# Performance work log

Hardware: AMD Instinct MI355X
Metric: run time of the kernel (lower is better)

## Reference

```python
import jax, jax.numpy as jnp
import numpy as np


def setup_inputs() -> dict:
    key = jax.random.key(0)
    k1, k2, k3, k4 = jax.random.split(key, 4)
    B, Cin, Cout, K, Wd, H, Wsp = 16, 256, 256, 3, 256, 64, 64
    fan_in = Cin * K * K
    return {
        "x": jax.random.normal(k1, (B, Cin, H, Wsp), dtype=jnp.float32),
        "w": jax.random.normal(k2, (B, Wd), dtype=jnp.float32),
        "conv_weight": jax.random.normal(k3, (Cout, Cin, K, K), dtype=jnp.float32) * 0.05,
        "style_w": jax.random.normal(k4, (Cin, Wd), dtype=jnp.float32) * 0.05,
        "style_b": jnp.zeros((Cin,), dtype=jnp.float32),
        "scale": jnp.asarray(1.0 / np.sqrt(fan_in), dtype=jnp.float32),
    }


def reference(x, w, conv_weight, style_w, style_b, scale):
    # x: [B, Cin, H, W]; w: [B, Wd]; conv_weight: [Cout, Cin, K, K]
    B, Cin, H, Wsp = x.shape
    Cout, _, K, _ = conv_weight.shape
    # style modulation: s = Linear(w) -> [B, 1, Cin, 1, 1]
    s = (w @ style_w.T + style_b).reshape(B, 1, Cin, 1, 1)
    # modulate + demodulate per-sample weights: [B, Cout, Cin, K, K]
    wt = (conv_weight * scale)[None] * s
    demod = jax.lax.rsqrt(jnp.sum(wt * wt, axis=(2, 3, 4), keepdims=True) + 1e-8)
    wt = (wt * demod).reshape(B * Cout, Cin, K, K)
    # grouped conv emulation: input [1, B*Cin, H, W], groups=B
    xr = x.reshape(1, B * Cin, H, Wsp)
    pad = 1
    out = jax.lax.conv_general_dilated(
        xr, wt,
        window_strides=(1, 1),
        padding=[(pad, pad), (pad, pad)],
        dimension_numbers=("NCHW", "OIHW", "NCHW"),
        feature_group_count=B,
    )
    return out.reshape(B, Cout, out.shape[2], out.shape[3])
```

## Files before the change

kernel.cpp:

```cpp
#include <hip/hip_runtime.h>
#include <hip/hip_bf16.h>

#define BB   16
#define CIN  256
#define COUT 256
#define WD   256
#define HH   64
#define WWS  64
#define NSP  4096
#define KW   9

typedef __attribute__((ext_vector_type(8))) short short8;
typedef __attribute__((ext_vector_type(4))) float f32x4;
typedef unsigned short ushort_t;
typedef unsigned int uint_t;

#define S_BYTES (BB*CIN*4)
#define WT_OFF (S_BYTES)
#define WT_BYTES (BB*9*COUT*CIN*2)
#define X_OFF (WT_OFF + WT_BYTES)
#define X_BYTES (BB*NSP*CIN*2)
#define ZP_OFF (X_OFF + X_BYTES)
#define ZP_BYTES 4096
#define WS_NEEDED ((size_t)(ZP_OFF + ZP_BYTES))

#define WAITVM0 asm volatile("s_waitcnt vmcnt(0)" ::: "memory")
#define WAITVM2 asm volatile("s_waitcnt vmcnt(2)" ::: "memory")

__device__ inline ushort_t f2bf(float f) {
    __hip_bfloat16 h = __float2bfloat16(f);
    return __builtin_bit_cast(ushort_t, h);
}

__device__ inline void gload_lds16(const ushort_t* g, ushort_t* l) {
    __builtin_amdgcn_global_load_lds(
        (const __attribute__((address_space(1))) void*)g,
        (__attribute__((address_space(3))) void*)l, 16, 0, 0);
}

__global__ __launch_bounds__(256)
void style_kernel(const float* __restrict__ w,
                  const float* __restrict__ style_w,
                  const float* __restrict__ style_b,
                  float* __restrict__ s) {
    const int b  = blockIdx.x;
    const int ci = threadIdx.x;
    __shared__ float wsh[WD];
    wsh[ci] = w[b * WD + ci];
    __syncthreads();
    const float* row = style_w + ci * WD;
    float acc = style_b[ci];
    #pragma unroll 4
    for (int k = 0; k < WD; ++k) acc += wsh[k] * row[k];
    s[b * CIN + ci] = acc;
}

__global__ __launch_bounds__(256)
void wt_kernel(const float* __restrict__ cw, const float* __restrict__ s,
               const float* __restrict__ scale_p, ushort_t* __restrict__ wt,
               float* __restrict__ zp) {
    const int co = blockIdx.x, b = blockIdx.y, ci = threadIdx.x;
    if (co == 0 && b == 0)
        ((float4*)zp)[ci] = make_float4(0.f, 0.f, 0.f, 0.f);
    const float sv = s[b * CIN + ci] * scale_p[0];
    const float* cp = cw + ((size_t)co * CIN + ci) * KW;
    float v[9];
    float ss = 0.f;
    #pragma unroll
    for (int t = 0; t < 9; ++t) { v[t] = cp[t] * sv; ss += v[t] * v[t]; }
    #pragma unroll
    for (int off = 32; off > 0; off >>= 1) ss += __shfl_down(ss, off);
    __shared__ float red[4];
    if ((ci & 63) == 0) red[ci >> 6] = ss;
    __syncthreads();
    const float dm = rsqrtf(red[0] + red[1] + red[2] + red[3] + 1e-8f);
    #pragma unroll
    for (int t = 0; t < 9; ++t)
        wt[((size_t)(b * 9 + t) * COUT + co) * CIN + ci] = f2bf(v[t] * dm);
}

__global__ __launch_bounds__(256)
void xpose_kernel(const float* __restrict__ x, ushort_t* __restrict__ xo) {
    const int spt = blockIdx.x;
    const int cit = blockIdx.y;
    const int b   = blockIdx.z;
    const int t   = threadIdx.x;
    __shared__ ushort_t tile[64 * 72];
    const int sp0 = spt * 64, ci0 = cit * 64;
    {
        const int spq = t & 15, cil = t >> 4;
        #pragma unroll
        for (int i = 0; i < 4; ++i) {
            const int ci = cil + i * 16;
            const float4 v = *(const float4*)(x + ((size_t)(b * CIN + ci0 + ci)) * NSP + sp0 + spq * 4);
            tile[(spq * 4 + 0) * 72 + ci] = f2bf(v.x);
            tile[(spq * 4 + 1) * 72 + ci] = f2bf(v.y);
            tile[(spq * 4 + 2) * 72 + ci] = f2bf(v.z);
            tile[(spq * 4 + 3) * 72 + ci] = f2bf(v.w);
        }
    }
    __syncthreads();
    {
        const int g8 = t & 7, sp = t >> 3;
        #pragma unroll
        for (int i = 0; i < 2; ++i) {
            const int spp = sp + i * 32;
            uint4 v = *(const uint4*)&tile[spp * 72 + g8 * 8];
            *(uint4*)(xo + ((size_t)(b * NSP + sp0 + spp)) * CIN + ci0 + g8 * 8) = v;
        }
    }
}

__global__ __launch_bounds__(256, 2)
void conv_mfma_kernel(const ushort_t* __restrict__ wt,
                      const ushort_t* __restrict__ xo,
                      const ushort_t* __restrict__ zp,
                      float* __restrict__ out) {
    const int wg     = blockIdx.x;
    const int b      = (wg & 7) | (((wg >> 3) & 1) << 3);
    const int cohalf = (wg >> 4) & 1;
    const int ntile  = wg >> 5;
    const int y0     = ntile * 4;

    const int tid  = threadIdx.x;
    const int lane = tid & 63;
    const int w    = tid >> 6;
    const int wm   = w >> 1;
    const int wn   = w & 1;
    const int wn2  = wn * 2;
    const int l15  = lane & 15;
    const int lg   = lane >> 4;

    __shared__ __align__(16) ushort_t lds_x[6 * 66 * 64];
    __shared__ __align__(16) ushort_t lds_a[3 * 128 * 32];

    const int srcqA = ((tid & 3) ^ ((tid >> 2) & 3)) * 8;
    const ushort_t* paDMA = wt + (size_t)b * (9 * COUT * CIN)
                          + (uint_t)(cohalf * 128 + (tid >> 2)) * CIN + srcqA;
    const ushort_t* xob = xo + (size_t)b * (NSP * CIN);

    const int sA8   = (lg ^ (l15 & 3)) * 8;
    const int abase = (wm * 64 + l15) * 32 + sA8;

    f32x4 acc[4][8];
    #pragma unroll
    for (int mi = 0; mi < 4; ++mi)
        #pragma unroll
        for (int ni = 0; ni < 8; ++ni) acc[mi][ni] = (f32x4){0.f, 0.f, 0.f, 0.f};

    if (tid < 96) {
        const int cell = tid >> 3;
        const int r = cell >> 1, c = (cell & 1) * 65;
        *(uint4*)&lds_x[(r * 66 + c) * 64 + (tid & 7) * 8] =
            make_uint4(0, 0, 0, 0);
    }

    #define STAGE_X(qt)                                                        \
    {   _Pragma("unroll")                                                      \
        for (int i_ = 0; i_ < 12; ++i_) {                                      \
            const int cell_ = i_ * 4 + w;                           \
            const int r_  = cell_ >> 3;                              \
            const int c0_ = 1 + (cell_ & 7) * 8;                               \
            const int y_  = y0 - 1 + r_;                                       \
            const int c_  = c0_ + (lane >> 3);                                 \
            const int qq_ = (lane & 7) ^ (c_ & 7);                             \
            const ushort_t* src_ = (y_ >= 0 && y_ < HH)                        \
                ? (xob + (uint_t)(y_ * WWS + c_ - 1) * CIN + (qt) * 64         \
                       + qq_ * 8)                                              \
                : (zp + lane * 8);                                             \
            gload_lds16(src_, lds_x + (r_ * 66 + c0_) * 64 + lane * 8);        \
        }                                                                      \
    }

    #define TAPB(ch2, t, BX, QB, QN)                                           \
    {                                                                          \
        WAITVM2;                          \
        __builtin_amdgcn_sched_barrier(0);                                     \
        __builtin_amdgcn_s_barrier();          \
        {                                 \
            const int lt2_ = (ch2) * 9 + (t) + 2;                              \
            const int tp_  = (lt2_ < 18) ? (lt2_ % 9) : (lt2_ - 18);           \
            const int cg_  = (lt2_ < 18) ? ((QB) + lt2_ / 9) : (QN);           \
            const uint_t ao_ = (uint_t)tp_ * 65536u + (uint_t)cg_ * 32u;       \
            ushort_t* ad_ = lds_a + (lt2_ % 3) * 4096 + tid * 8;               \
            gload_lds16(paDMA + ao_, ad_);                                     \
            gload_lds16(paDMA + 16384 + ao_, ad_ + 2048);                      \
        }                                                                      \
        const int ky_ = (t) / 3, kx_ = (t) % 3;                                \
        const ushort_t* ab_ = lds_a + (((ch2) * 9 + (t)) % 3) * 4096 + abase;  \
        short8 af_[4];                                                         \
        _Pragma("unroll")                                                      \
        for (int mi_ = 0; mi_ < 4; ++mi_)                                      \
            af_[mi_] = *(const short8*)(ab_ + mi_ * 512);                      \
        short8 bf_[8];                                                         \
        _Pragma("unroll")                                                      \
        for (int ni_ = 0; ni_ < 8; ++ni_)                                      \
            bf_[ni_] = *(const short8*)(lds_x + BX[kx_]                        \
                        + (((ni_ >> 2) + ky_) * 66) * 64 + (ni_ & 3) * 1024);  \
        __builtin_amdgcn_s_setprio(1);                                         \
        _Pragma("unroll")                                                      \
        for (int mi_ = 0; mi_ < 4; ++mi_)                                      \
            _Pragma("unroll")                                                  \
            for (int ni_ = 0; ni_ < 8; ++ni_)                                  \
                acc[mi_][ni_] = __builtin_amdgcn_mfma_f32_16x16x32_bf16(       \
                    bf_[ni_], af_[mi_], acc[mi_][ni_], 0, 0, 0);               \
        __builtin_amdgcn_s_setprio(0);                                         \
        __builtin_amdgcn_sched_barrier(0);                                     \
    }

    STAGE_X(0);
    gload_lds16(paDMA, lds_a + tid * 8);
    gload_lds16(paDMA + 16384, lds_a + 2048 + tid * 8);
    gload_lds16(paDMA + 65536, lds_a + 4096 + tid * 8);
    gload_lds16(paDMA + 65536 + 16384, lds_a + 6144 + tid * 8);
    WAITVM0;
    asm volatile("s_waitcnt lgkmcnt(0)" ::: "memory");
    __builtin_amdgcn_sched_barrier(0);
    __builtin_amdgcn_s_barrier();

    #pragma unroll 1
    for (int qt = 0; qt < 4; ++qt) {
        if (qt) {
            asm volatile("s_waitcnt lgkmcnt(0)" ::: "memory");
            __builtin_amdgcn_sched_barrier(0);
            __builtin_amdgcn_s_barrier();
            STAGE_X(qt);
            WAITVM0;
            __builtin_amdgcn_sched_barrier(0);
            __builtin_amdgcn_s_barrier();
        }
        const int qb = qt * 2;
        const int qn = ((qt + 1) & 3) * 2;

        int bx0[3], bx1[3];
        #pragma unroll
        for (int kx = 0; kx < 3; ++kx) {
            const int colb = (wn2 * 66 + l15 + kx) * 64;
            const int k7   = (l15 + kx) & 7;
            bx0[kx] = colb + ((0 + lg) ^ k7) * 8;
            bx1[kx] = colb + ((4 + lg) ^ k7) * 8;
        }

        TAPB(0,0,bx0,qb,qn) TAPB(0,1,bx0,qb,qn) TAPB(0,2,bx0,qb,qn)
        TAPB(0,3,bx0,qb,qn) TAPB(0,4,bx0,qb,qn) TAPB(0,5,bx0,qb,qn)
        TAPB(0,6,bx0,qb,qn) TAPB(0,7,bx0,qb,qn) TAPB(0,8,bx0,qb,qn)
        TAPB(1,0,bx1,qb,qn) TAPB(1,1,bx1,qb,qn) TAPB(1,2,bx1,qb,qn)
        TAPB(1,3,bx1,qb,qn) TAPB(1,4,bx1,qb,qn) TAPB(1,5,bx1,qb,qn)
        TAPB(1,6,bx1,qb,qn) TAPB(1,7,bx1,qb,qn) TAPB(1,8,bx1,qb,qn)
    }
    #undef TAPB
    #undef STAGE_X

    asm volatile("s_waitcnt vmcnt(0) lgkmcnt(0)" ::: "memory");
    __builtin_amdgcn_sched_barrier(0);

    #pragma unroll
    for (int mi = 0; mi < 4; ++mi) {
        const int co = cohalf * 128 + wm * 64 + mi * 16 + l15;
        float* ob = out + ((size_t)(b * COUT + co)) * NSP
                  + ntile * 256 + wn * 128 + lg * 4;
        #pragma unroll
        for (int ni = 0; ni < 8; ++ni)
            *(f32x4*)(ob + (ni >> 2) * 64 + (ni & 3) * 16) = acc[mi][ni];
    }
}

__global__ __launch_bounds__(256)
void modconv_kernel(const float* __restrict__ x,
                    const float* __restrict__ cw,
                    const float* __restrict__ s,
                    const float* __restrict__ scale_p,
                    float* __restrict__ out) {
    const int tile = blockIdx.x;
    const int co   = blockIdx.y;
    const int b    = blockIdx.z;
    const int tid  = threadIdx.x;
    const float scale = scale_p[0];

    __shared__ float s_wt[CIN * KW];
    __shared__ float s_x[18 * 66];
    __shared__ float red[4];

    const float* cwb = cw + (size_t)co * CIN * KW;
    const float* sb  = s + b * CIN;
    float sumsq = 0.f;
    for (int i = tid; i < CIN * KW; i += 256) {
        float v = cwb[i] * scale * sb[i / KW];
        s_wt[i] = v;
        sumsq += v * v;
    }
    #pragma unroll
    for (int off = 32; off > 0; off >>= 1) sumsq += __shfl_down(sumsq, off);
    if ((tid & 63) == 0) red[tid >> 6] = sumsq;
    __syncthreads();
    const float demod = rsqrtf(red[0] + red[1] + red[2] + red[3] + 1e-8f);
    for (int i = tid; i < CIN * KW; i += 256) s_wt[i] *= demod;

    const int tx = tid & 63;
    const int tr = tid >> 6;
    const int y0 = tile * 16;
    float acc[4] = {0.f, 0.f, 0.f, 0.f};

    for (int ci = 0; ci < CIN; ++ci) {
        __syncthreads();
        const float* xb = x + ((size_t)(b * CIN + ci)) * (HH * WWS);
        for (int idx = tid; idx < 18 * 66; idx += 256) {
            const int r = idx / 66, c = idx % 66;
            const int yg = y0 - 1 + r, xg = c - 1;
            float v = 0.f;
            if (yg >= 0 && yg < HH && xg >= 0 && xg < WWS) v = xb[yg * WWS + xg];
            s_x[idx] = v;
        }
        __syncthreads();
        const float* wr = s_wt + ci * KW;
        const float w0 = wr[0], w1 = wr[1], w2 = wr[2];
        const float w3 = wr[3], w4 = wr[4], w5 = wr[5];
        const float w6 = wr[6], w7 = wr[7], w8 = wr[8];
        const int rbase = tr * 4;
        float xv[6][3];
        #pragma unroll
        for (int j = 0; j < 6; ++j)
            #pragma unroll
            for (int k = 0; k < 3; ++k) xv[j][k] = s_x[(rbase + j) * 66 + tx + k];
        #pragma unroll
        for (int i = 0; i < 4; ++i)
            acc[i] += w0 * xv[i][0] + w1 * xv[i][1] + w2 * xv[i][2]
                    + w3 * xv[i+1][0] + w4 * xv[i+1][1] + w5 * xv[i+1][2]
                    + w6 * xv[i+2][0] + w7 * xv[i+2][1] + w8 * xv[i+2][2];
    }
    float* ob = out + (((size_t)(b * COUT + co)) * HH + y0) * WWS + tx;
    #pragma unroll
    for (int i = 0; i < 4; ++i) ob[(tr * 4 + i) * WWS] = acc[i];
}

extern "C" void kernel_launch(void* const* d_in, const int* in_sizes, int n_in,
                              void* d_out, int out_size, void* d_ws, size_t ws_size,
                              hipStream_t stream) {
    const float* x       = (const float*)d_in[0];
    const float* w       = (const float*)d_in[1];
    const float* cw      = (const float*)d_in[2];
    const float* style_w = (const float*)d_in[3];
    const float* style_b = (const float*)d_in[4];
    const float* scale_p = (const float*)d_in[5];
    float*       out     = (float*)d_out;

    float*    s    = (float*)d_ws;
    ushort_t* wswt = (ushort_t*)((char*)d_ws + WT_OFF);
    ushort_t* wsx  = (ushort_t*)((char*)d_ws + X_OFF);
    float*    zp   = (float*)((char*)d_ws + ZP_OFF);

    style_kernel<<<dim3(BB), 256, 0, stream>>>(w, style_w, style_b, s);

    if (ws_size >= WS_NEEDED) {
        wt_kernel<<<dim3(COUT, BB), 256, 0, stream>>>(cw, s, scale_p, wswt, zp);
        xpose_kernel<<<dim3(64, 4, BB), 256, 0, stream>>>(x, wsx);
        conv_mfma_kernel<<<dim3(512), 256, 0, stream>>>(wswt, wsx,
                                                        (const ushort_t*)zp, out);
    } else {
        modconv_kernel<<<dim3(4, COUT, BB), 256, 0, stream>>>(x, cw, s, scale_p, out);
    }
}
```

Before: 109.8 us.

## Widen conv tile to all 256 output channels and double-buffer LDS fragment reads

Each workgroup now computes all 256 output channels for its spatial tile instead of half of them. This halves the grid to 256 blocks and doubles the per-wave accumulator tile to 8x8 MFMA fragments, so each staged input tile is reused across twice as many channels and is no longer loaded twice. A and B fragments are register double-buffered, so reads for the next tap are issued before the current tap's MFMAs. The weight DMA is issued before the wait, with the vmcnt threshold raised to match the larger loads. The costs are much higher register pressure (launch bounds drop to one block per CU), lower occupancy, and fewer workgroups than a 256-CU device can fill with more than one block each.

```diff
diff --git a/kernel.cpp b/kernel.cpp
--- a/kernel.cpp
+++ b/kernel.cpp
@@ -25,7 +25,7 @@
 #define WS_NEEDED ((size_t)(ZP_OFF + ZP_BYTES))
 
 #define WAITVM0 asm volatile("s_waitcnt vmcnt(0)" ::: "memory")
-#define WAITVM2 asm volatile("s_waitcnt vmcnt(2)" ::: "memory")
+#define WAITVM4 asm volatile("s_waitcnt vmcnt(4)" ::: "memory")
 
 __device__ inline ushort_t f2bf(float f) {
     __hip_bfloat16 h = __float2bfloat16(f);
@@ -111,16 +111,15 @@
     }
 }
 
-__global__ __launch_bounds__(256, 2)
+__global__ __launch_bounds__(256, 1)
 void conv_mfma_kernel(const ushort_t* __restrict__ wt,
                       const ushort_t* __restrict__ xo,
                       const ushort_t* __restrict__ zp,
                       float* __restrict__ out) {
-    const int wg     = blockIdx.x;
-    const int b      = (wg & 7) | (((wg >> 3) & 1) << 3);
-    const int cohalf = (wg >> 4) & 1;
-    const int ntile  = wg >> 5;
-    const int y0     = ntile * 4;
+    const int wg    = blockIdx.x;
+    const int b     = (wg & 7) | (((wg >> 3) & 1) << 3);
+    const int ntile = wg >> 4;
+    const int y0    = ntile * 4;
 
     const int tid  = threadIdx.x;
     const int lane = tid & 63;
@@ -132,21 +131,32 @@
     const int lg   = lane >> 4;
 
     __shared__ __align__(16) ushort_t lds_x[6 * 66 * 64];
-    __shared__ __align__(16) ushort_t lds_a[3 * 128 * 32];
+    __shared__ __align__(16) ushort_t lds_a[3 * 256 * 32];
 
     const int srcqA = ((tid & 3) ^ ((tid >> 2) & 3)) * 8;
     const ushort_t* paDMA = wt + (size_t)b * (9 * COUT * CIN)
-                          + (uint_t)(cohalf * 128 + (tid >> 2)) * CIN + srcqA;
+                          + (uint_t)(tid >> 2) * CIN + srcqA;
     const ushort_t* xob = xo + (size_t)b * (NSP * CIN);
 
     const int sA8   = (lg ^ (l15 & 3)) * 8;
-    const int abase = (wm * 64 + l15) * 32 + sA8;
-
-    f32x4 acc[4][8];
-    #pragma unroll
-    for (int mi = 0; mi < 4; ++mi)
+    const int abase = (wm * 128 + l15) * 32 + sA8;
+
+    int bx[2][3];
+    #pragma unroll
+    for (int c4 = 0; c4 < 2; ++c4)
+        #pragma unroll
+        for (int kx = 0; kx < 3; ++kx) {
+            const int k7 = (l15 + kx) & 7;
+            bx[c4][kx] = (wn2 * 66 + l15 + kx) * 64 + ((c4 * 4 + lg) ^ k7) * 8;
+        }
+
+    f32x4 acc[8][8];
+    #pragma unroll
+    for (int mi = 0; mi < 8; ++mi)
         #pragma unroll
         for (int ni = 0; ni < 8; ++ni) acc[mi][ni] = (f32x4){0.f, 0.f, 0.f, 0.f};
+
+    short8 afr[2][8], bfr[2][8];
 
     if (tid < 96) {
         const int cell = tid >> 3;
@@ -172,91 +182,106 @@
         }                                                                      \
     }
 
-    #define TAPB(ch2, t, BX, QB, QN)                                           \
+    #define ISSUE_A(tp, cg, buf)                                               \
+    {   const ushort_t* as_ = paDMA + (tp) * 65536 + (cg) * 32;                \
+        ushort_t* ad_ = lds_a + (buf) * 8192 + tid * 8;                        \
+        gload_lds16(as_,          ad_);                                        \
+        gload_lds16(as_ + 16384,  ad_ + 2048);                                 \
+        gload_lds16(as_ + 32768,  ad_ + 4096);                                 \
+        gload_lds16(as_ + 49152,  ad_ + 6144);                                 \
+    }
+
+    #define TAPP(q2, t, qb, qn)                                                \
     {                                                                          \
-        WAITVM2;                          \
+        constexpr int u_ = (q2) * 9 + (t);                          \
+        constexpr int P_ = u_ & 1;                                             \
+        constexpr int Q_ = P_ ^ 1;                                             \
+        {                                                    \
+            constexpr int lt2_ = u_ + 2;                                       \
+            constexpr int tp_  = (lt2_ < 18) ? (lt2_ % 9) : (lt2_ - 18);       \
+            const int cg_ = (lt2_ < 18) ? ((qb) + lt2_ / 9) : (qn);            \
+            ISSUE_A(tp_, cg_, lt2_ % 3);                                       \
+        }                                                                      \
+        WAITVM4;                                        \
         __builtin_amdgcn_sched_barrier(0);                                     \
-        __builtin_amdgcn_s_barrier();          \
-        {                                 \
-            const int lt2_ = (ch2) * 9 + (t) + 2;                              \
-            const int tp_  = (lt2_ < 18) ? (lt2_ % 9) : (lt2_ - 18);           \
-            const int cg_  = (lt2_ < 18) ? ((QB) + lt2_ / 9) : (QN);           \
-            const uint_t ao_ = (uint_t)tp_ * 65536u + (uint_t)cg_ * 32u;       \
-            ushort_t* ad_ = lds_a + (lt2_ % 3) * 4096 + tid * 8;               \
-            gload_lds16(paDMA + ao_, ad_);                                     \
-            gload_lds16(paDMA + 16384 + ao_, ad_ + 2048);                      \
+        __builtin_amdgcn_s_barrier();           \
+        {                                       \
+            const ushort_t* ar_ = lds_a + ((u_ + 1) % 3) * 8192 + abase;       \
+            _Pragma("unroll")                                                  \
+            for (int mi_ = 0; mi_ < 8; ++mi_)                                  \
+                afr[Q_][mi_] = *(const short8*)(ar_ + mi_ * 512);              \
         }                                                                      \
-        const int ky_ = (t) / 3, kx_ = (t) % 3;                                \
-        const ushort_t* ab_ = lds_a + (((ch2) * 9 + (t)) % 3) * 4096 + abase;  \
-        short8 af_[4];                                                         \
-        _Pragma("unroll")                                                      \
-        for (int mi_ = 0; mi_ < 4; ++mi_)                                      \
-            af_[mi_] = *(const short8*)(ab_ + mi_ * 512);                      \
-        short8 bf_[8];                                                         \
-        _Pragma("unroll")                                                      \
-        for (int ni_ = 0; ni_ < 8; ++ni_)                                      \
-            bf_[ni_] = *(const short8*)(lds_x + BX[kx_]                        \
-                        + (((ni_ >> 2) + ky_) * 66) * 64 + (ni_ & 3) * 1024);  \
+        if constexpr (u_ < 17) {                \
+            constexpr int u1_ = u_ + 1;                                        \
+            constexpr int t1_ = u1_ % 9;                                       \
+            constexpr int c1_ = u1_ / 9;                                       \
+            constexpr int ky_ = t1_ / 3, kx_ = t1_ % 3;                        \
+            _Pragma("unroll")                                                  \
+            for (int ni_ = 0; ni_ < 8; ++ni_)                                  \
+                bfr[Q_][ni_] = *(const short8*)(lds_x + bx[c1_][kx_]           \
+                    + (((ni_ >> 2) + ky_) * 66) * 64 + (ni_ & 3) * 1024);      \
+        }                                                                      \
         __builtin_amdgcn_s_setprio(1);                                         \
         _Pragma("unroll")                                                      \
-        for (int mi_ = 0; mi_ < 4; ++mi_)                                      \
+        for (int mi_ = 0; mi_ < 8; ++mi_)                                      \
             _Pragma("unroll")                                                  \
             for (int ni_ = 0; ni_ < 8; ++ni_)                                  \
                 acc[mi_][ni_] = __builtin_amdgcn_mfma_f32_16x16x32_bf16(       \
-                    bf_[ni_], af_[mi_], acc[mi_][ni_], 0, 0, 0);               \
+                    bfr[P_][ni_], afr[P_][mi_], acc[mi_][ni_], 0, 0, 0);       \
         __builtin_amdgcn_s_setprio(0);                                         \
         __builtin_amdgcn_sched_barrier(0);                                     \
     }
 
     STAGE_X(0);
-    gload_lds16(paDMA, lds_a + tid * 8);
-    gload_lds16(paDMA + 16384, lds_a + 2048 + tid * 8);
-    gload_lds16(paDMA + 65536, lds_a + 4096 + tid * 8);
-    gload_lds16(paDMA + 65536 + 16384, lds_a + 6144 + tid * 8);
+    ISSUE_A(0, 0, 0);
+    ISSUE_A(1, 0, 1);
     WAITVM0;
     asm volatile("s_waitcnt lgkmcnt(0)" ::: "memory");
     __builtin_amdgcn_sched_barrier(0);
     __builtin_amdgcn_s_barrier();
+    {
+        const ushort_t* ar = lds_a + abase;
+        #pragma unroll
+        for (int mi = 0; mi < 8; ++mi) afr[0][mi] = *(const short8*)(ar + mi * 512);
+        #pragma unroll
+        for (int ni = 0; ni < 8; ++ni)
+            bfr[0][ni] = *(const short8*)(lds_x + bx[0][0]
+                          + ((ni >> 2) * 66) * 64 + (ni & 3) * 1024);
+    }
 
     #pragma unroll 1
     for (int qt = 0; qt < 4; ++qt) {
         if (qt) {
-            asm volatile("s_waitcnt lgkmcnt(0)" ::: "memory");
-            __builtin_amdgcn_sched_barrier(0);
             __builtin_amdgcn_s_barrier();
             STAGE_X(qt);
             WAITVM0;
             __builtin_amdgcn_sched_barrier(0);
             __builtin_amdgcn_s_barrier();
+            #pragma unroll
+            for (int ni = 0; ni < 8; ++ni)
+                bfr[0][ni] = *(const short8*)(lds_x + bx[0][0]
+                              + ((ni >> 2) * 66) * 64 + (ni & 3) * 1024);
         }
         const int qb = qt * 2;
         const int qn = ((qt + 1) & 3) * 2;
 
-        int bx0[3], bx1[3];
-        #pragma unroll
-        for (int kx = 0; kx < 3; ++kx) {
-            const int colb = (wn2 * 66 + l15 + kx) * 64;
-            const int k7   = (l15 + kx) & 7;
-            bx0[kx] = colb + ((0 + lg) ^ k7) * 8;
-            bx1[kx] = colb + ((4 + lg) ^ k7) * 8;
-        }
-
-        TAPB(0,0,bx0,qb,qn) TAPB(0,1,bx0,qb,qn) TAPB(0,2,bx0,qb,qn)
-        TAPB(0,3,bx0,qb,qn) TAPB(0,4,bx0,qb,qn) TAPB(0,5,bx0,qb,qn)
-        TAPB(0,6,bx0,qb,qn) TAPB(0,7,bx0,qb,qn) TAPB(0,8,bx0,qb,qn)
-        TAPB(1,0,bx1,qb,qn) TAPB(1,1,bx1,qb,qn) TAPB(1,2,bx1,qb,qn)
-        TAPB(1,3,bx1,qb,qn) TAPB(1,4,bx1,qb,qn) TAPB(1,5,bx1,qb,qn)
-        TAPB(1,6,bx1,qb,qn) TAPB(1,7,bx1,qb,qn) TAPB(1,8,bx1,qb,qn)
-    }
-    #undef TAPB
+        TAPP(0,0,qb,qn) TAPP(0,1,qb,qn) TAPP(0,2,qb,qn)
+        TAPP(0,3,qb,qn) TAPP(0,4,qb,qn) TAPP(0,5,qb,qn)
+        TAPP(0,6,qb,qn) TAPP(0,7,qb,qn) TAPP(0,8,qb,qn)
+        TAPP(1,0,qb,qn) TAPP(1,1,qb,qn) TAPP(1,2,qb,qn)
+        TAPP(1,3,qb,qn) TAPP(1,4,qb,qn) TAPP(1,5,qb,qn)
+        TAPP(1,6,qb,qn) TAPP(1,7,qb,qn) TAPP(1,8,qb,qn)
+    }
+    #undef TAPP
+    #undef ISSUE_A
     #undef STAGE_X
 
     asm volatile("s_waitcnt vmcnt(0) lgkmcnt(0)" ::: "memory");
     __builtin_amdgcn_sched_barrier(0);
 
     #pragma unroll
-    for (int mi = 0; mi < 4; ++mi) {
-        const int co = cohalf * 128 + wm * 64 + mi * 16 + l15;
+    for (int mi = 0; mi < 8; ++mi) {
+        const int co = wm * 128 + mi * 16 + l15;
         float* ob = out + ((size_t)(b * COUT + co)) * NSP
                   + ntile * 256 + wn * 128 + lg * 4;
         #pragma unroll
@@ -354,7 +379,7 @@
     if (ws_size >= WS_NEEDED) {
         wt_kernel<<<dim3(COUT, BB), 256, 0, stream>>>(cw, s, scale_p, wswt, zp);
         xpose_kernel<<<dim3(64, 4, BB), 256, 0, stream>>>(x, wsx);
-        conv_mfma_kernel<<<dim3(512), 256, 0, stream>>>(wswt, wsx,
+        conv_mfma_kernel<<<dim3(256), 256, 0, stream>>>(wswt, wsx,
                                                         (const ushort_t*)zp, out);
     } else {
         modconv_kernel<<<dim3(4, COUT, BB), 256, 0, stream>>>(x, cw, s, scale_p, out);
```

New measurement: 112.9 us. +2.8%, slower.
